# Optimization experiments

Measured on AMD Instinct MI355X. Metric: run time of the kernel, lower is better.

## Reference

```python
import jax, jax.numpy as jnp
import numpy as np

N_RES = 30000
N_ATOMS = 6
N_EDGES = 300000
HIDDEN = 128
N_GRAPHS = 32
CENTRAL_IDX = 1
EPS = 1e-6


def _normalize(x, axis=-1):
    # matches torch F.normalize (eps=1e-12 on the norm)
    return x / jnp.maximum(jnp.linalg.norm(x, axis=axis, keepdims=True), 1e-12)


def _rbf(D, D_min=0.0, D_max=20.0, num_rbf=16):
    mu = jnp.linspace(D_min, D_max, num_rbf)
    sigma = (D_max - D_min) / num_rbf
    return jnp.exp(-(((D[..., None] - mu) / sigma) ** 2))


def _quaternions(R):
    Rxx, Ryy, Rzz = R[:, 0, 0], R[:, 1, 1], R[:, 2, 2]
    mag = 0.5 * jnp.sqrt(jnp.abs(1.0 + jnp.stack([Rxx - Ryy - Rzz, -Rxx + Ryy - Rzz, -Rxx - Ryy + Rzz], -1)))
    signs = jnp.sign(jnp.stack([R[:, 2, 1] - R[:, 1, 2], R[:, 0, 2] - R[:, 2, 0], R[:, 1, 0] - R[:, 0, 1]], -1))
    xyz = signs * mag
    w = jnp.sqrt(jax.nn.relu(1.0 + Rxx + Ryy + Rzz))[:, None] / 2.0
    return _normalize(jnp.concatenate([xyz, w], -1))


def _layernorm(x, w, b, eps=1e-5):
    mu = x.mean(-1, keepdims=True)
    var = ((x - mu) ** 2).mean(-1, keepdims=True)
    return (x - mu) / jnp.sqrt(var + eps) * w + b


def _forward(coords, central_coords, node_W, node_b, node_ln_w, node_ln_b,
             edge_W, edge_b, edge_ln_w, edge_ln_b, batch, edge_index):
    n_res, n_atoms = coords.shape[:2]
    L = n_res * n_atoms
    src, tgt = edge_index[0], edge_index[1]

    # chain-boundary masks (replace torch's NaN-write + nan_to_num with masking to 0)
    boundary = jnp.concatenate([jnp.zeros(1, bool), batch[1:] != batch[:-1]])      # first res of new graph
    boundary_next = jnp.concatenate([boundary[1:], jnp.zeros(1, bool)])            # last res of a graph

    Xf = coords.reshape(-1, 3)
    ar = jnp.arange(L)
    col = jnp.arange(n_atoms)

    # ---- dihedral ----
    U = _normalize(Xf[1:] - Xf[:-1])
    c1 = _normalize(jnp.cross(U[:-2], U[1:-1]))
    c2 = _normalize(jnp.cross(U[1:-1], U[2:]))
    dih = jnp.arccos(jnp.clip((c1 * c2).sum(-1), -1.0 + EPS, 1.0 - EPS)) * jnp.sign((c2 * U[:-2]).sum(-1))
    dih = jnp.pad(dih, (1, 2)).reshape(n_res, n_atoms)
    d_mask = ((ar > 0) & (ar < L - 2)).reshape(n_res, n_atoms)
    d_mask = d_mask & ~(boundary[:, None] & (col == 0)[None])
    d_mask = d_mask & ~(boundary_next[:, None] & (col >= n_atoms - 2)[None])
    dih_feat = jnp.where(d_mask[..., None], jnp.stack([jnp.sin(dih), jnp.cos(dih)], -1), 0.0).reshape(n_res, -1)

    # ---- bond angle ----
    dX0 = _normalize(Xf[:-2] - Xf[1:-1])
    dX1 = _normalize(Xf[2:] - Xf[1:-1])
    cosang = (dX0 * dX1).sum(-1)
    sinang = jnp.sqrt(1.0 - cosang ** 2 + EPS)
    cosang = jnp.pad(cosang, (1, 1)).reshape(n_res, n_atoms)
    sinang = jnp.pad(sinang, (1, 1)).reshape(n_res, n_atoms)
    a_mask = ((ar > 0) & (ar < L - 1)).reshape(n_res, n_atoms)
    a_mask = a_mask & ~(boundary[:, None] & (col == 0)[None])
    a_mask = a_mask & ~(boundary_next[:, None] & (col == n_atoms - 1)[None])
    ang_feat = jnp.where(a_mask[..., None], jnp.stack([sinang, cosang], -1), 0.0).reshape(n_res, -1)

    # ---- local frame Q ----
    cX = central_coords
    du = _normalize(cX[1:] - cX[:-1])
    bvec = _normalize(du[:-1] - du[1:])
    nvec = _normalize(jnp.cross(du[:-1], du[1:]))
    Q = jnp.stack([bvec, nvec, jnp.cross(bvec, nvec)], -1)          # [n_res-2, 3, 3]
    Q = jnp.pad(Q, ((1, 1), (0, 0), (0, 0)))
    r = jnp.arange(n_res)
    q_valid = (r > 0) & (r < n_res - 1) & (~boundary) & (~boundary_next)
    Q = Q * q_valid[:, None, None]                                   # invalid frames -> 0 (== nan_to_num result)

    # ---- relative orientation quaternion per edge ----
    R = jnp.einsum('eki,ekj->eij', Q[tgt], Q[src])                   # tgt_Q^T @ src_Q
    orient = jnp.where((q_valid[src] & q_valid[tgt])[:, None], _quaternions(R), 0.0)

    # ---- inter distances / directions (edge) ----
    diff = coords[src][:, None, :, :] - coords[tgt][:, :, None, :]   # [E, n_atoms_t, n_atoms_s, 3]
    inter_D = jnp.sqrt((diff ** 2).sum(-1) + EPS)
    inter_dist = _rbf(inter_D).reshape(diff.shape[0], -1)            # [E, 576]
    inter_direct = jnp.einsum('eki,etsk->etsi', Q[tgt], _normalize(diff)).reshape(diff.shape[0], -1)  # [E, 108]

    # ---- intra distances / directions (node) ----
    keep = np.arange(n_atoms) != CENTRAL_IDX
    d_nc = coords[:, keep] - cX[:, None]                             # [n_res, 5, 3]
    intra_dist = jnp.log(jnp.sqrt((d_nc ** 2).sum(-1) + EPS))        # [n_res, 5]
    intra_direct = jnp.einsum('rki,rak->rai', Q, _normalize(d_nc)).reshape(n_res, -1)  # [n_res, 15]

    h_V = jnp.concatenate([dih_feat, ang_feat, intra_dist, intra_direct], -1)  # [n_res, 44]
    h_E = jnp.concatenate([orient, inter_dist, inter_direct], -1)              # [E, 688]
    h_V = _layernorm(h_V @ node_W + node_b, node_ln_w, node_ln_b)
    h_E = _layernorm(h_E @ edge_W + edge_b, edge_ln_w, edge_ln_b)
    return h_V, h_E


def setup_inputs() -> dict:
    key = jax.random.key(0)
    ks = jax.random.split(key, 8)
    coords = jax.random.normal(ks[0], (N_RES, N_ATOMS, 3), jnp.float32)
    central_coords = jax.random.normal(ks[1], (N_RES, 3), jnp.float32)
    batch = jnp.sort(jax.random.randint(ks[2], (N_RES,), 0, N_GRAPHS))
    edge_index = jax.random.randint(ks[3], (2, N_EDGES), 0, N_RES)
    node_W = jax.random.normal(ks[4], (44, HIDDEN), jnp.float32) / np.sqrt(44.0)
    edge_W = jax.random.normal(ks[5], (688, HIDDEN), jnp.float32) / np.sqrt(688.0)
    return {
        'coords': coords, 'central_coords': central_coords,
        'node_W': node_W, 'node_b': jnp.zeros((HIDDEN,), jnp.float32),
        'node_ln_w': jnp.ones((HIDDEN,), jnp.float32), 'node_ln_b': jnp.zeros((HIDDEN,), jnp.float32),
        'edge_W': edge_W, 'edge_b': jnp.zeros((HIDDEN,), jnp.float32),
        'edge_ln_w': jnp.ones((HIDDEN,), jnp.float32), 'edge_ln_b': jnp.zeros((HIDDEN,), jnp.float32),
        'batch': batch, 'edge_index': edge_index,
    }


def reference(coords, central_coords, node_W, node_b, node_ln_w, node_ln_b,
              edge_W, edge_b, edge_ln_w, edge_ln_b, batch, edge_index):
    return _forward(coords, central_coords, node_W, node_b, node_ln_w, node_ln_b,
                    edge_W, edge_b, edge_ln_w, edge_ln_b, batch, edge_index)
```

## Files before the change

### kernel.cpp

```cpp
#include <hip/hip_runtime.h>
#include <hip/hip_bf16.h>


#define N_RES   30000
#define N_ATOMS 6
#define LFLAT   (N_RES * N_ATOMS)
#define N_EDGES 300000
#define HID     128
#define NODE_IN 44
#define EDGE_IN 688
#define KSTEPS  43
#define KS_A    32
#define EPSF    1e-6f
#define LN_EPS  1e-5f
#define MTILE   32

typedef unsigned short ushort_t;
typedef short short8 __attribute__((ext_vector_type(8)));
typedef float float16v __attribute__((ext_vector_type(16)));

static __device__ __forceinline__ unsigned short f2bf(float x) {
    __hip_bfloat16 h = __float2bfloat16(x);
    unsigned short u;
    __builtin_memcpy(&u, &h, 2);
    return u;
}

struct F3 { float x, y, z; };
static __device__ __forceinline__ F3 ld3(const float* p, long idx) {
    F3 r; r.x = p[idx*3+0]; r.y = p[idx*3+1]; r.z = p[idx*3+2]; return r;
}
static __device__ __forceinline__ F3 subv(F3 a, F3 b) { return {a.x-b.x, a.y-b.y, a.z-b.z}; }
static __device__ __forceinline__ float dotv(F3 a, F3 b) { return a.x*b.x + a.y*b.y + a.z*b.z; }
static __device__ __forceinline__ F3 crossv(F3 a, F3 b) {
    return {a.y*b.z - a.z*b.y, a.z*b.x - a.x*b.z, a.x*b.y - a.y*b.x};
}
static __device__ __forceinline__ F3 nrmv(F3 a) {
    float inv = rsqrtf(fmaxf(dotv(a, a), 1e-24f));
    return {a.x*inv, a.y*inv, a.z*inv};
}
static __device__ __forceinline__ float sgn(float x) { return (x > 0.f) ? 1.f : ((x < 0.f) ? -1.f : 0.f); }

__global__ void k_packw(const float* __restrict__ W, unsigned short* __restrict__ Wp) {
    int s = blockIdx.x;
    int tid = threadIdx.x;
    int w = tid >> 6, lane = tid & 63;
    int ch = w * 32 + (lane & 31);
    int kh = lane >> 5;
    uint4 out;
    uint u[4];
    #pragma unroll
    for (int jp = 0; jp < 4; ++jp) {
        unsigned int lohi[2];
        #pragma unroll
        for (int b = 0; b < 2; ++b) {
            int jj = 2 * jp + b;
            int kn = 16 * s + kh * 8 + jj;
            int ko = (kn < 684) ? (kn + 4) : (kn - 684);
            lohi[b] = f2bf(W[(long)ko * HID + ch]);
        }
        u[jp] = lohi[0] | (lohi[1] << 16);
    }
    out.x = u[0]; out.y = u[1]; out.z = u[2]; out.w = u[3];
    *(uint4*)(Wp + ((size_t)(s * 4 + w) * 64 + lane) * 8) = out;
}

__global__ void k_frames(const float* __restrict__ central, const int* __restrict__ batch,
                         float* __restrict__ Qbuf, int* __restrict__ qval) {
    int r = blockIdx.x * 256 + threadIdx.x;
    if (r >= N_RES) return;
    bool bnd   = (r > 0)         && (batch[r]   != batch[r-1]);
    bool bndn  = (r < N_RES - 1) && (batch[r+1] != batch[r]);
    bool valid = (r > 0) && (r < N_RES - 1) && !bnd && !bndn;
    float Q[9] = {0,0,0,0,0,0,0,0,0};
    if (valid) {
        F3 cp = ld3(central, (long)r-1), cc = ld3(central, (long)r), cn = ld3(central, (long)r+1);
        F3 u0 = nrmv(subv(cc, cp));
        F3 u1 = nrmv(subv(cn, cc));
        F3 b  = nrmv(subv(u0, u1));
        F3 n  = nrmv(crossv(u0, u1));
        F3 c  = crossv(b, n);
        Q[0]=b.x; Q[1]=n.x; Q[2]=c.x;
        Q[3]=b.y; Q[4]=n.y; Q[5]=c.y;
        Q[6]=b.z; Q[7]=n.z; Q[8]=c.z;
    }
    #pragma unroll
    for (int k = 0; k < 9; k++) Qbuf[(size_t)r*9 + k] = Q[k];
    qval[r] = valid ? 1 : 0;
}

__global__ __launch_bounds__(HID) void k_node(
    const float* __restrict__ coords, const float* __restrict__ central,
    const float* __restrict__ node_W, const float* __restrict__ node_b,
    const float* __restrict__ lnw, const float* __restrict__ lnb,
    const int* __restrict__ batch, const float* __restrict__ Qbuf,
    float* __restrict__ out) {
    int r = blockIdx.x;
    int tid = threadIdx.x;
    __shared__ float feat[NODE_IN];
    __shared__ float red[4];

    if (tid < 6) {
        int c = tid;
        long j = (long)r * N_ATOMS + c;
        bool bnd  = (r > 0)         && (batch[r]   != batch[r-1]);
        bool bndn = (r < N_RES - 1) && (batch[r+1] != batch[r]);
        float sd = 0.f, cd = 0.f;
        bool dm = (j > 0) && (j < LFLAT - 2) && !(bnd && c == 0) && !(bndn && c >= N_ATOMS - 2);
        if (dm) {
            F3 x0 = ld3(coords, j-1), x1 = ld3(coords, j), x2 = ld3(coords, j+1), x3 = ld3(coords, j+2);
            F3 u1 = nrmv(subv(x1, x0)), u2 = nrmv(subv(x2, x1)), u3 = nrmv(subv(x3, x2));
            F3 c1 = nrmv(crossv(u1, u2)), c2 = nrmv(crossv(u2, u3));
            float cc = fminf(fmaxf(dotv(c1, c2), -1.f + EPSF), 1.f - EPSF);
            float s  = sgn(dotv(c2, u1));
            sd = s * sqrtf(fmaxf(1.f - cc*cc, 0.f));
            cd = (s != 0.f) ? cc : 1.f;
        }
        feat[2*c] = sd; feat[2*c+1] = cd;
        float sa = 0.f, ca = 0.f;
        bool am = (j > 0) && (j < LFLAT - 1) && !(bnd && c == 0) && !(bndn && c == N_ATOMS - 1);
        if (am) {
            F3 x0 = ld3(coords, j-1), x1 = ld3(coords, j), x2 = ld3(coords, j+1);
            F3 d0 = nrmv(subv(x0, x1)), d1 = nrmv(subv(x2, x1));
            float cv = dotv(d0, d1);
            float t = 1.f - cv*cv + EPSF;
            sa = t * rsqrtf(t);
            ca = cv;
        }
        feat[12 + 2*c] = sa; feat[12 + 2*c + 1] = ca;
    } else if (tid < 11) {
        int a = tid - 6;
        int atom = (a == 0) ? 0 : (a + 1);
        F3 x  = ld3(coords, (long)r * N_ATOMS + atom);
        F3 cx = ld3(central, (long)r);
        F3 d  = subv(x, cx);
        float d2 = dotv(d, d);
        feat[24 + a] = 0.5f * __logf(d2 + EPSF);
        float inv = rsqrtf(fmaxf(d2, 1e-24f));
        float nx = d.x*inv, ny = d.y*inv, nz = d.z*inv;
        const float* Q = Qbuf + (size_t)r * 9;
        #pragma unroll
        for (int i = 0; i < 3; i++)
            feat[29 + a*3 + i] = Q[0+i]*nx + Q[3+i]*ny + Q[6+i]*nz;
    }
    __syncthreads();

    float acc = node_b[tid];
    #pragma unroll
    for (int i = 0; i < NODE_IN; i++)
        acc += feat[i] * node_W[(long)i * HID + tid];

    float s = acc;
    #pragma unroll
    for (int m = 1; m < 64; m <<= 1) s += __shfl_xor(s, m, 64);
    int wv = tid >> 6;
    if ((tid & 63) == 0) red[wv] = s;
    __syncthreads();
    float mu = (red[0] + red[1]) * (1.f / HID);
    float dv = acc - mu;
    float q = dv * dv;
    #pragma unroll
    for (int m = 1; m < 64; m <<= 1) q += __shfl_xor(q, m, 64);
    if ((tid & 63) == 0) red[2 + wv] = q;
    __syncthreads();
    float var = (red[2] + red[3]) * (1.f / HID);
    float y = dv * rsqrtf(var + LN_EPS) * lnw[tid] + lnb[tid];
    out[(size_t)r * HID + tid] = y;
}

__global__ __launch_bounds__(256, 4) void k_edge(
    const float* __restrict__ coords, const int* __restrict__ eidx,
    const unsigned short* __restrict__ Wpack, const float* __restrict__ edge_b,
    const float* __restrict__ lnw, const float* __restrict__ lnb,
    const float* __restrict__ Qbuf, const int* __restrict__ qval,
    float* __restrict__ outE) {
    __shared__ __align__(16) unsigned char smemA[KS_A * 64 * 8 * 2];
    __shared__ float cS[64][18];
    __shared__ float qtS[MTILE][9];
    __shared__ int sS[MTILE], tS[MTILE];

    unsigned short* Ast = (unsigned short*)smemA;
    int tid = threadIdx.x;
    int lane = tid & 63;
    int w = tid >> 6;
    int e0 = blockIdx.x * MTILE;

    if (tid < MTILE) {
        sS[tid] = eidx[e0 + tid];
        tS[tid] = eidx[N_EDGES + e0 + tid];
    }
    __syncthreads();

    #pragma unroll
    for (int it = 0; it < 5; ++it) {
        int idx = tid + it * 256;
        if (idx < 64 * 18) {
            int slot = idx / 18;
            int rem  = idx - slot * 18;
            int res  = (slot < 32) ? sS[slot] : tS[slot - 32];
            cS[slot][rem] = coords[(size_t)res * 18 + rem];
        }
    }

    uint2 qpk;
    if (tid < MTILE) {
        int s = sS[tid];
        int t = tS[tid];
        float Qs[9], Qt[9];
        #pragma unroll
        for (int k = 0; k < 9; k++) {
            Qs[k] = Qbuf[(size_t)s*9 + k];
            Qt[k] = Qbuf[(size_t)t*9 + k];
            qtS[tid][k] = Qt[k];
        }
        float R[9];
        #pragma unroll
        for (int i = 0; i < 3; i++)
            #pragma unroll
            for (int jj = 0; jj < 3; jj++)
                R[i*3+jj] = Qt[0+i]*Qs[0+jj] + Qt[3+i]*Qs[3+jj] + Qt[6+i]*Qs[6+jj];
        float m0 = 0.5f * sqrtf(fabsf(1.f + R[0] - R[4] - R[8]));
        float m1 = 0.5f * sqrtf(fabsf(1.f - R[0] + R[4] - R[8]));
        float m2 = 0.5f * sqrtf(fabsf(1.f - R[0] - R[4] + R[8]));
        float xq = sgn(R[7] - R[5]) * m0;
        float yq = sgn(R[2] - R[6]) * m1;
        float zq = sgn(R[3] - R[1]) * m2;
        float wq = 0.5f * sqrtf(fmaxf(1.f + R[0] + R[4] + R[8], 0.f));
        float nq2 = xq*xq + yq*yq + zq*zq + wq*wq;
        float inv = rsqrtf(fmaxf(nq2, 1e-24f));
        float vm = (qval[s] && qval[t]) ? 1.f : 0.f;
        qpk.x = f2bf(xq * inv * vm) | ((unsigned int)f2bf(yq * inv * vm) << 16);
        qpk.y = f2bf(zq * inv * vm) | ((unsigned int)f2bf(wq * inv * vm) << 16);
    }
    __syncthreads();

    int e  = tid & 31;
    int p0 = tid >> 5;

    float vdir[4][3];
    #pragma unroll
    for (int it = 0; it < 4; ++it) {
        int pair = p0 + 8 * it;
        int ta = pair / 6, sa = pair - ta * 6;
        float dx = cS[e][sa*3+0] - cS[32+e][ta*3+0];
        float dy = cS[e][sa*3+1] - cS[32+e][ta*3+1];
        float dz = cS[e][sa*3+2] - cS[32+e][ta*3+2];
        float d2 = dx*dx + dy*dy + dz*dz;
        float t  = d2 + EPSF;
        float D  = t * rsqrtf(t);
        float a8 = D * 0.8f;
        unsigned int u[8];
        #pragma unroll
        for (int i = 0; i < 8; i++) {
            float z0 = a8 - (float)(2*i)     * 1.06666672f;
            float z1 = a8 - (float)(2*i + 1) * 1.06666672f;
            u[i] = f2bf(__expf(-(z0*z0))) | ((unsigned int)f2bf(__expf(-(z1*z1))) << 16);
        }
        uint4 lo; lo.x = u[0]; lo.y = u[1]; lo.z = u[2]; lo.w = u[3];
        uint4 hi; hi.x = u[4]; hi.y = u[5]; hi.z = u[6]; hi.w = u[7];
        *(uint4*)(Ast + (pair * 64 + e) * 8)      = lo;
        *(uint4*)(Ast + (pair * 64 + 32 + e) * 8) = hi;
        float inv = rsqrtf(fmaxf(d2, 1e-24f));
        float nx = dx*inv, ny = dy*inv, nz = dz*inv;
        #pragma unroll
        for (int i = 0; i < 3; i++)
            vdir[it][i] = qtS[e][0+i]*nx + qtS[e][3+i]*ny + qtS[e][6+i]*nz;
    }
    __syncthreads();

    float16v acc;
    #pragma unroll
    for (int i = 0; i < 16; i++) acc[i] = 0.f;
    const short8* Ap = (const short8*)smemA;
    const short8* Bp = (const short8*)Wpack;
    for (int s = 0; s < KS_A; ++s) {
        short8 a = Ap[s * 64 + lane];
        short8 b = Bp[(s * 4 + w) * 64 + lane];
        acc = __builtin_amdgcn_mfma_f32_32x32x16_bf16(a, b, acc, 0, 0, 0);
    }
    __syncthreads();

    if (tid < 128) {
        int e2 = tid & 31;
        int pair = 32 + (tid >> 5);
        int ta = pair / 6, sa = pair - ta * 6;
        float dx = cS[e2][sa*3+0] - cS[32+e2][ta*3+0];
        float dy = cS[e2][sa*3+1] - cS[32+e2][ta*3+1];
        float dz = cS[e2][sa*3+2] - cS[32+e2][ta*3+2];
        float d2 = dx*dx + dy*dy + dz*dz;
        float t  = d2 + EPSF;
        float D  = t * rsqrtf(t);
        float a8 = D * 0.8f;
        unsigned int u[8];
        #pragma unroll
        for (int i = 0; i < 8; i++) {
            float z0 = a8 - (float)(2*i)     * 1.06666672f;
            float z1 = a8 - (float)(2*i + 1) * 1.06666672f;
            u[i] = f2bf(__expf(-(z0*z0))) | ((unsigned int)f2bf(__expf(-(z1*z1))) << 16);
        }
        uint4 lo; lo.x = u[0]; lo.y = u[1]; lo.z = u[2]; lo.w = u[3];
        uint4 hi; hi.x = u[4]; hi.y = u[5]; hi.z = u[6]; hi.w = u[7];
        int lks = pair - 32;
        *(uint4*)(Ast + (lks * 64 + e2) * 8)      = lo;
        *(uint4*)(Ast + (lks * 64 + 32 + e2) * 8) = hi;
        float inv = rsqrtf(fmaxf(d2, 1e-24f));
        float nx = dx*inv, ny = dy*inv, nz = dz*inv;
        #pragma unroll
        for (int i = 0; i < 3; i++) {
            float v = qtS[e2][0+i]*nx + qtS[e2][3+i]*ny + qtS[e2][6+i]*nz;
            int kn = 576 + pair * 3 + i;
            int s2 = kn >> 4, r2 = kn & 15;
            Ast[(((s2 - 32) * 64) + (r2 >> 3) * 32 + e2) * 8 + (r2 & 7)] = f2bf(v);
        }
    }
    #pragma unroll
    for (int it = 0; it < 4; ++it) {
        int pair = p0 + 8 * it;
        #pragma unroll
        for (int i = 0; i < 3; i++) {
            int kn = 576 + pair * 3 + i;
            int s2 = kn >> 4, r2 = kn & 15;
            Ast[(((s2 - 32) * 64) + (r2 >> 3) * 32 + e) * 8 + (r2 & 7)] = f2bf(vdir[it][i]);
        }
    }
    if (tid < MTILE)
        *(uint2*)(Ast + ((10 * 64 + 32 + tid) * 8 + 4)) = qpk;
    __syncthreads();

    for (int s = KS_A; s < KSTEPS; ++s) {
        short8 a = Ap[(s - KS_A) * 64 + lane];
        short8 b = Bp[(s * 4 + w) * 64 + lane];
        acc = __builtin_amdgcn_mfma_f32_32x32x16_bf16(a, b, acc, 0, 0, 0);
    }

    __syncthreads();
    float* C_s = (float*)smemA;
    int col = lane & 31;
    #pragma unroll
    for (int r = 0; r < 16; ++r) {
        int row = (r & 3) + 8 * (r >> 2) + 4 * (lane >> 5);
        C_s[row * 132 + w * 32 + col] = acc[r];
    }
    __syncthreads();

    int ee = tid >> 3;
    int p  = tid & 7;
    const float* Crow = C_s + ee * 132 + p * 16;
    float x[16];
    float sum = 0.f;
    #pragma unroll
    for (int j = 0; j < 16; ++j) {
        x[j] = Crow[j] + edge_b[p * 16 + j];
        sum += x[j];
    }
    #pragma unroll
    for (int m = 1; m < 8; m <<= 1) sum += __shfl_xor(sum, m, 64);
    float mu = sum * (1.f / HID);
    float vs = 0.f;
    #pragma unroll
    for (int j = 0; j < 16; ++j) { float d = x[j] - mu; vs += d * d; }
    #pragma unroll
    for (int m = 1; m < 8; m <<= 1) vs += __shfl_xor(vs, m, 64);
    float is = rsqrtf(vs * (1.f / HID) + LN_EPS);
    float* op = outE + (size_t)(e0 + ee) * HID + p * 16;
    #pragma unroll
    for (int j = 0; j < 16; ++j) {
        int ch = p * 16 + j;
        op[j] = (x[j] - mu) * is * lnw[ch] + lnb[ch];
    }
}

extern "C" void kernel_launch(void* const* d_in, const int* in_sizes, int n_in,
                              void* d_out, int out_size, void* d_ws, size_t ws_size,
                              hipStream_t stream) {
    (void)in_sizes; (void)n_in; (void)out_size; (void)ws_size;
    const float* coords  = (const float*)d_in[0];
    const float* central = (const float*)d_in[1];
    const float* node_W  = (const float*)d_in[2];
    const float* node_b  = (const float*)d_in[3];
    const float* node_lw = (const float*)d_in[4];
    const float* node_lb = (const float*)d_in[5];
    const float* edge_W  = (const float*)d_in[6];
    const float* edge_b  = (const float*)d_in[7];
    const float* edge_lw = (const float*)d_in[8];
    const float* edge_lb = (const float*)d_in[9];
    const int*   batch   = (const int*)d_in[10];
    const int*   eidx    = (const int*)d_in[11];

    unsigned short* Wpack = (unsigned short*)d_ws;
    float* Qbuf = (float*)((char*)d_ws + (size_t)EDGE_IN * HID * 2);
    int*   qval = (int*)(Qbuf + (size_t)N_RES * 9);

    float* outV = (float*)d_out;
    float* outE = outV + (size_t)N_RES * HID;

    hipLaunchKernelGGL(k_packw,  dim3(KSTEPS),            dim3(256), 0, stream, edge_W, Wpack);
    hipLaunchKernelGGL(k_frames, dim3((N_RES + 255)/256), dim3(256), 0, stream, central, batch, Qbuf, qval);
    hipLaunchKernelGGL(k_node,   dim3(N_RES),             dim3(HID), 0, stream,
                       coords, central, node_W, node_b, node_lw, node_lb, batch, Qbuf, outV);
    hipLaunchKernelGGL(k_edge,   dim3(N_EDGES / MTILE),   dim3(256), 0, stream,
                       coords, eidx, Wpack, edge_b, edge_lw, edge_lb, Qbuf, qval, outE);
}
```

Measured before the change: 339.3 us.

## Batch residues per node block and compute all edge RBF tasks before MFMA

The node kernel now handles 16 residues per 256-thread block. It stages node_W, the LN params and neighbouring coordinates in shared memory, so the weights are loaded once per block instead of once per residue, and features are built by 176 threads in parallel. In the edge kernel the leftover RBF pairs (32-35) are computed before the first MFMA loop by the idle p0<4 threads and written to shared memory after that loop, spreading the work across all warps. The cost is more LDS per node block (about 23KB for the weights), which lowers occupancy, plus extra live registers in the edge kernel. The direction normalisation now uses rsqrt(d2+eps) instead of rsqrt(max(d2,1e-24)), a slight numeric change.

```diff
diff --git a/kernel.cpp b/kernel.cpp
--- a/kernel.cpp
+++ b/kernel.cpp
@@ -14,8 +14,8 @@
 #define EPSF    1e-6f
 #define LN_EPS  1e-5f
 #define MTILE   32
-
-typedef unsigned short ushort_t;
+#define RPB     16
+
 typedef short short8 __attribute__((ext_vector_type(8)));
 typedef float float16v __attribute__((ext_vector_type(16)));
 
@@ -29,6 +29,9 @@
 struct F3 { float x, y, z; };
 static __device__ __forceinline__ F3 ld3(const float* p, long idx) {
     F3 r; r.x = p[idx*3+0]; r.y = p[idx*3+1]; r.z = p[idx*3+2]; return r;
+}
+static __device__ __forceinline__ F3 ldl(const float* p, int a) {
+    F3 r; r.x = p[a*3+0]; r.y = p[a*3+1]; r.z = p[a*3+2]; return r;
 }
 static __device__ __forceinline__ F3 subv(F3 a, F3 b) { return {a.x-b.x, a.y-b.y, a.z-b.z}; }
 static __device__ __forceinline__ float dotv(F3 a, F3 b) { return a.x*b.x + a.y*b.y + a.z*b.z; }
@@ -89,83 +92,103 @@
     qval[r] = valid ? 1 : 0;
 }
 
-__global__ __launch_bounds__(HID) void k_node(
+__global__ __launch_bounds__(256, 4) void k_node(
     const float* __restrict__ coords, const float* __restrict__ central,
     const float* __restrict__ node_W, const float* __restrict__ node_b,
     const float* __restrict__ lnw, const float* __restrict__ lnb,
     const int* __restrict__ batch, const float* __restrict__ Qbuf,
     float* __restrict__ out) {
-    int r = blockIdx.x;
+    __shared__ float Wlds[NODE_IN * HID];
+    __shared__ float feat[RPB][NODE_IN];
+    __shared__ float cst[(RPB + 2) * 18];
+    __shared__ float bS[HID], lwS[HID], lbS[HID];
+    __shared__ float red[8];
+
     int tid = threadIdx.x;
-    __shared__ float feat[NODE_IN];
-    __shared__ float red[4];
-
-    if (tid < 6) {
-        int c = tid;
-        long j = (long)r * N_ATOMS + c;
+    int r0 = blockIdx.x * RPB;
+
+    for (int i = tid; i < NODE_IN * HID; i += 256) Wlds[i] = node_W[i];
+    if (tid < HID) { bS[tid] = node_b[tid]; lwS[tid] = lnw[tid]; lbS[tid] = lnb[tid]; }
+    for (int i = tid; i < (RPB + 2) * 18; i += 256) {
+        long g = (long)(r0 - 1) * 18 + i;
+        cst[i] = (g >= 0 && g < (long)N_RES * 18) ? coords[g] : 0.f;
+    }
+    __syncthreads();
+
+    if (tid < RPB * 11) {
+        int rl = tid / 11, role = tid - rl * 11;
+        int r = r0 + rl;
         bool bnd  = (r > 0)         && (batch[r]   != batch[r-1]);
         bool bndn = (r < N_RES - 1) && (batch[r+1] != batch[r]);
-        float sd = 0.f, cd = 0.f;
-        bool dm = (j > 0) && (j < LFLAT - 2) && !(bnd && c == 0) && !(bndn && c >= N_ATOMS - 2);
-        if (dm) {
-            F3 x0 = ld3(coords, j-1), x1 = ld3(coords, j), x2 = ld3(coords, j+1), x3 = ld3(coords, j+2);
-            F3 u1 = nrmv(subv(x1, x0)), u2 = nrmv(subv(x2, x1)), u3 = nrmv(subv(x3, x2));
-            F3 c1 = nrmv(crossv(u1, u2)), c2 = nrmv(crossv(u2, u3));
-            float cc = fminf(fmaxf(dotv(c1, c2), -1.f + EPSF), 1.f - EPSF);
-            float s  = sgn(dotv(c2, u1));
-            sd = s * sqrtf(fmaxf(1.f - cc*cc, 0.f));
-            cd = (s != 0.f) ? cc : 1.f;
-        }
-        feat[2*c] = sd; feat[2*c+1] = cd;
-        float sa = 0.f, ca = 0.f;
-        bool am = (j > 0) && (j < LFLAT - 1) && !(bnd && c == 0) && !(bndn && c == N_ATOMS - 1);
-        if (am) {
-            F3 x0 = ld3(coords, j-1), x1 = ld3(coords, j), x2 = ld3(coords, j+1);
-            F3 d0 = nrmv(subv(x0, x1)), d1 = nrmv(subv(x2, x1));
-            float cv = dotv(d0, d1);
-            float t = 1.f - cv*cv + EPSF;
-            sa = t * rsqrtf(t);
-            ca = cv;
-        }
-        feat[12 + 2*c] = sa; feat[12 + 2*c + 1] = ca;
-    } else if (tid < 11) {
-        int a = tid - 6;
-        int atom = (a == 0) ? 0 : (a + 1);
-        F3 x  = ld3(coords, (long)r * N_ATOMS + atom);
-        F3 cx = ld3(central, (long)r);
-        F3 d  = subv(x, cx);
-        float d2 = dotv(d, d);
-        feat[24 + a] = 0.5f * __logf(d2 + EPSF);
-        float inv = rsqrtf(fmaxf(d2, 1e-24f));
-        float nx = d.x*inv, ny = d.y*inv, nz = d.z*inv;
-        const float* Q = Qbuf + (size_t)r * 9;
-        #pragma unroll
-        for (int i = 0; i < 3; i++)
-            feat[29 + a*3 + i] = Q[0+i]*nx + Q[3+i]*ny + Q[6+i]*nz;
-    }
-    __syncthreads();
-
-    float acc = node_b[tid];
-    #pragma unroll
-    for (int i = 0; i < NODE_IN; i++)
-        acc += feat[i] * node_W[(long)i * HID + tid];
-
-    float s = acc;
-    #pragma unroll
-    for (int m = 1; m < 64; m <<= 1) s += __shfl_xor(s, m, 64);
-    int wv = tid >> 6;
-    if ((tid & 63) == 0) red[wv] = s;
-    __syncthreads();
-    float mu = (red[0] + red[1]) * (1.f / HID);
-    float dv = acc - mu;
-    float q = dv * dv;
-    #pragma unroll
-    for (int m = 1; m < 64; m <<= 1) q += __shfl_xor(q, m, 64);
-    if ((tid & 63) == 0) red[2 + wv] = q;
-    __syncthreads();
-    float var = (red[2] + red[3]) * (1.f / HID);
-    float y = dv * rsqrtf(var + LN_EPS) * lnw[tid] + lnb[tid];
-    out[(size_t)r * HID + tid] = y;
+        const float* C = cst + (rl + 1) * 18;
+        if (role < 6) {
+            int c = role;
+            long j = (long)r * N_ATOMS + c;
+            float sd = 0.f, cd = 0.f;
+            bool dm = (j > 0) && (j < LFLAT - 2) && !(bnd && c == 0) && !(bndn && c >= N_ATOMS - 2);
+            if (dm) {
+                F3 x0 = ldl(C, c-1), x1 = ldl(C, c), x2 = ldl(C, c+1), x3 = ldl(C, c+2);
+                F3 u1 = nrmv(subv(x1, x0)), u2 = nrmv(subv(x2, x1)), u3 = nrmv(subv(x3, x2));
+                F3 c1 = nrmv(crossv(u1, u2)), c2 = nrmv(crossv(u2, u3));
+                float cc = fminf(fmaxf(dotv(c1, c2), -1.f + EPSF), 1.f - EPSF);
+                float s  = sgn(dotv(c2, u1));
+                sd = s * sqrtf(fmaxf(1.f - cc*cc, 0.f));
+                cd = (s != 0.f) ? cc : 1.f;
+            }
+            feat[rl][2*c] = sd; feat[rl][2*c+1] = cd;
+            float sa = 0.f, ca = 0.f;
+            bool am = (j > 0) && (j < LFLAT - 1) && !(bnd && c == 0) && !(bndn && c == N_ATOMS - 1);
+            if (am) {
+                F3 x0 = ldl(C, c-1), x1 = ldl(C, c), x2 = ldl(C, c+1);
+                F3 d0 = nrmv(subv(x0, x1)), d1 = nrmv(subv(x2, x1));
+                float cv = dotv(d0, d1);
+                float t = 1.f - cv*cv + EPSF;
+                sa = t * rsqrtf(t);
+                ca = cv;
+            }
+            feat[rl][12 + 2*c] = sa; feat[rl][12 + 2*c + 1] = ca;
+        } else {
+            int a = role - 6;
+            int atom = (a == 0) ? 0 : (a + 1);
+            F3 x  = ldl(C, atom);
+            F3 cx = ld3(central, (long)r);
+            F3 d  = subv(x, cx);
+            float d2 = dotv(d, d);
+            feat[rl][24 + a] = 0.5f * __logf(d2 + EPSF);
+            float inv = rsqrtf(fmaxf(d2, 1e-24f));
+            float nx = d.x*inv, ny = d.y*inv, nz = d.z*inv;
+            const float* Q = Qbuf + (size_t)r * 9;
+            #pragma unroll
+            for (int i = 0; i < 3; i++)
+                feat[rl][29 + a*3 + i] = Q[0+i]*nx + Q[3+i]*ny + Q[6+i]*nz;
+        }
+    }
+    __syncthreads();
+
+    int ch = tid & 127;
+    int g  = tid >> 7;
+    int w  = tid >> 6;
+    for (int it = 0; it < 8; ++it) {
+        int rl = it * 2 + g;
+        float acc = bS[ch];
+        #pragma unroll
+        for (int i = 0; i < NODE_IN; i++)
+            acc += feat[rl][i] * Wlds[i * HID + ch];
+        float s = acc;
+        #pragma unroll
+        for (int m = 1; m < 64; m <<= 1) s += __shfl_xor(s, m, 64);
+        if ((tid & 63) == 0) red[w] = s;
+        __syncthreads();
+        float mu = (red[2*g] + red[2*g+1]) * (1.f / HID);
+        float dv = acc - mu;
+        float q = dv * dv;
+        #pragma unroll
+        for (int m = 1; m < 64; m <<= 1) q += __shfl_xor(q, m, 64);
+        if ((tid & 63) == 0) red[4 + w] = q;
+        __syncthreads();
+        float var = (red[4 + 2*g] + red[4 + 2*g + 1]) * (1.f / HID);
+        out[(size_t)(r0 + rl) * HID + ch] = dv * rsqrtf(var + LN_EPS) * lwS[ch] + lbS[ch];
+    }
 }
 
 __global__ __launch_bounds__(256, 4) void k_edge(
@@ -226,8 +249,7 @@
         float yq = sgn(R[2] - R[6]) * m1;
         float zq = sgn(R[3] - R[1]) * m2;
         float wq = 0.5f * sqrtf(fmaxf(1.f + R[0] + R[4] + R[8], 0.f));
-        float nq2 = xq*xq + yq*yq + zq*zq + wq*wq;
-        float inv = rsqrtf(fmaxf(nq2, 1e-24f));
+        float inv = rsqrtf(fmaxf(xq*xq + yq*yq + zq*zq + wq*wq, 1e-24f));
         float vm = (qval[s] && qval[t]) ? 1.f : 0.f;
         qpk.x = f2bf(xq * inv * vm) | ((unsigned int)f2bf(yq * inv * vm) << 16);
         qpk.y = f2bf(zq * inv * vm) | ((unsigned int)f2bf(wq * inv * vm) << 16);
@@ -237,34 +259,45 @@
     int e  = tid & 31;
     int p0 = tid >> 5;
 
+    #define RBF_TASK(PAIR, EV, ULO, UHI, DIR)                                        \
+    {                                                                                \
+        int ta = (PAIR) / 6, sa = (PAIR) - ta * 6;                                   \
+        float dx = cS[EV][sa*3+0] - cS[32+(EV)][ta*3+0];                             \
+        float dy = cS[EV][sa*3+1] - cS[32+(EV)][ta*3+1];                             \
+        float dz = cS[EV][sa*3+2] - cS[32+(EV)][ta*3+2];                             \
+        float d2 = dx*dx + dy*dy + dz*dz;                                            \
+        float t  = d2 + EPSF;                                                        \
+        float inv = rsqrtf(t);                                                       \
+        float a8 = t * inv * 0.8f;                             \
+        unsigned int uu[8];                                                          \
+        _Pragma("unroll")                                                            \
+        for (int i = 0; i < 8; i++) {                                                \
+            float z0 = a8 - (float)(2*i)     * 1.06666672f;                          \
+            float z1 = a8 - (float)(2*i + 1) * 1.06666672f;                          \
+            uu[i] = f2bf(__expf(-(z0*z0))) |                                         \
+                    ((unsigned int)f2bf(__expf(-(z1*z1))) << 16);                    \
+        }                                                                            \
+        ULO.x = uu[0]; ULO.y = uu[1]; ULO.z = uu[2]; ULO.w = uu[3];                  \
+        UHI.x = uu[4]; UHI.y = uu[5]; UHI.z = uu[6]; UHI.w = uu[7];                  \
+        float nx = dx*inv, ny = dy*inv, nz = dz*inv;                                 \
+        _Pragma("unroll")                                                            \
+        for (int i = 0; i < 3; i++)                                                  \
+            DIR[i] = qtS[EV][0+i]*nx + qtS[EV][3+i]*ny + qtS[EV][6+i]*nz;            \
+    }
+
     float vdir[4][3];
     #pragma unroll
     for (int it = 0; it < 4; ++it) {
         int pair = p0 + 8 * it;
-        int ta = pair / 6, sa = pair - ta * 6;
-        float dx = cS[e][sa*3+0] - cS[32+e][ta*3+0];
-        float dy = cS[e][sa*3+1] - cS[32+e][ta*3+1];
-        float dz = cS[e][sa*3+2] - cS[32+e][ta*3+2];
-        float d2 = dx*dx + dy*dy + dz*dz;
-        float t  = d2 + EPSF;
-        float D  = t * rsqrtf(t);
-        float a8 = D * 0.8f;
-        unsigned int u[8];
-        #pragma unroll
-        for (int i = 0; i < 8; i++) {
-            float z0 = a8 - (float)(2*i)     * 1.06666672f;
-            float z1 = a8 - (float)(2*i + 1) * 1.06666672f;
-            u[i] = f2bf(__expf(-(z0*z0))) | ((unsigned int)f2bf(__expf(-(z1*z1))) << 16);
-        }
-        uint4 lo; lo.x = u[0]; lo.y = u[1]; lo.z = u[2]; lo.w = u[3];
-        uint4 hi; hi.x = u[4]; hi.y = u[5]; hi.z = u[6]; hi.w = u[7];
+        uint4 lo, hi;
+        RBF_TASK(pair, e, lo, hi, vdir[it]);
         *(uint4*)(Ast + (pair * 64 + e) * 8)      = lo;
         *(uint4*)(Ast + (pair * 64 + 32 + e) * 8) = hi;
-        float inv = rsqrtf(fmaxf(d2, 1e-24f));
-        float nx = dx*inv, ny = dy*inv, nz = dz*inv;
-        #pragma unroll
-        for (int i = 0; i < 3; i++)
-            vdir[it][i] = qtS[e][0+i]*nx + qtS[e][3+i]*ny + qtS[e][6+i]*nz;
+    }
+    uint4 lo5, hi5;
+    float vdir5[3];
+    if (p0 < 4) {
+        RBF_TASK(32 + p0, e, lo5, hi5, vdir5);
     }
     __syncthreads();
 
@@ -280,37 +313,14 @@
     }
     __syncthreads();
 
-    if (tid < 128) {
-        int e2 = tid & 31;
-        int pair = 32 + (tid >> 5);
-        int ta = pair / 6, sa = pair - ta * 6;
-        float dx = cS[e2][sa*3+0] - cS[32+e2][ta*3+0];
-        float dy = cS[e2][sa*3+1] - cS[32+e2][ta*3+1];
-        float dz = cS[e2][sa*3+2] - cS[32+e2][ta*3+2];
-        float d2 = dx*dx + dy*dy + dz*dz;
-        float t  = d2 + EPSF;
-        float D  = t * rsqrtf(t);
-        float a8 = D * 0.8f;
-        unsigned int u[8];
-        #pragma unroll
-        for (int i = 0; i < 8; i++) {
-            float z0 = a8 - (float)(2*i)     * 1.06666672f;
-            float z1 = a8 - (float)(2*i + 1) * 1.06666672f;
-            u[i] = f2bf(__expf(-(z0*z0))) | ((unsigned int)f2bf(__expf(-(z1*z1))) << 16);
-        }
-        uint4 lo; lo.x = u[0]; lo.y = u[1]; lo.z = u[2]; lo.w = u[3];
-        uint4 hi; hi.x = u[4]; hi.y = u[5]; hi.z = u[6]; hi.w = u[7];
-        int lks = pair - 32;
-        *(uint4*)(Ast + (lks * 64 + e2) * 8)      = lo;
-        *(uint4*)(Ast + (lks * 64 + 32 + e2) * 8) = hi;
-        float inv = rsqrtf(fmaxf(d2, 1e-24f));
-        float nx = dx*inv, ny = dy*inv, nz = dz*inv;
+    if (p0 < 4) {
+        *(uint4*)(Ast + (p0 * 64 + e) * 8)      = lo5;
+        *(uint4*)(Ast + (p0 * 64 + 32 + e) * 8) = hi5;
         #pragma unroll
         for (int i = 0; i < 3; i++) {
-            float v = qtS[e2][0+i]*nx + qtS[e2][3+i]*ny + qtS[e2][6+i]*nz;
-            int kn = 576 + pair * 3 + i;
+            int kn = 576 + (32 + p0) * 3 + i;
             int s2 = kn >> 4, r2 = kn & 15;
-            Ast[(((s2 - 32) * 64) + (r2 >> 3) * 32 + e2) * 8 + (r2 & 7)] = f2bf(v);
+            Ast[(((s2 - 32) * 64) + (r2 >> 3) * 32 + e) * 8 + (r2 & 7)] = f2bf(vdir5[i]);
         }
     }
     #pragma unroll
@@ -396,7 +406,7 @@
 
     hipLaunchKernelGGL(k_packw,  dim3(KSTEPS),            dim3(256), 0, stream, edge_W, Wpack);
     hipLaunchKernelGGL(k_frames, dim3((N_RES + 255)/256), dim3(256), 0, stream, central, batch, Qbuf, qval);
-    hipLaunchKernelGGL(k_node,   dim3(N_RES),             dim3(HID), 0, stream,
+    hipLaunchKernelGGL(k_node,   dim3(N_RES / RPB),       dim3(256), 0, stream,
                        coords, central, node_W, node_b, node_lw, node_lb, batch, Qbuf, outV);
     hipLaunchKernelGGL(k_edge,   dim3(N_EDGES / MTILE),   dim3(256), 0, stream,
                        coords, eidx, Wpack, edge_b, edge_lw, edge_lb, Qbuf, qval, outE);
```

New measurement: 346.6 us. 1.02x slower.
